# Performance work log

Measured on AMD Instinct MI355X. Metric: run time of the kernel, lower is better.

The kernel has to match this reference:

```python
import jax, jax.numpy as jnp
import numpy as np

D_K = 64

def setup_inputs() -> dict:
    key = jax.random.key(0)
    k1, k2, k3 = jax.random.split(key, 3)
    B, H, S, d = 4, 16, 2048, D_K
    Q = jax.random.normal(k1, (B, H, S, d), dtype=jnp.float32)
    K = jax.random.normal(k2, (B, H, S, d), dtype=jnp.float32)
    V = jax.random.normal(k3, (B, H, S, d), dtype=jnp.float32)
    attn_mask = jnp.ones((1, 1, S, S), dtype=jnp.float32)
    return {"Q": Q, "K": K, "V": V, "attn_mask": attn_mask}

def reference(Q, K, V, attn_mask):
    # scores = Q K^T / sqrt(d_k)  -> [B, H, S, S]
    scale = 1.0 / np.sqrt(D_K).astype(np.float32)
    scores = jnp.einsum('bhqd,bhkd->bhqk', Q, K) * scale
    # unnormalized exp (NO max-subtraction, faithful to original)
    scores = jnp.exp(scores)
    # multiplicative mask applied POST-exp
    scores = scores * attn_mask
    # manual sum-normalization with eps
    attn = scores / (jnp.sum(scores, axis=-1, keepdims=True) + 1e-08)
    context = jnp.einsum('bhqk,bhkd->bhqd', attn, V)
    return (context, attn)
```

## Files before the change

kernel.cpp:

```cpp
#include <hip/hip_runtime.h>

#define S_LEN 2048
#define D_KD  64
#define NKT   32
#define NBH   64

typedef __attribute__((ext_vector_type(8))) short short8;
typedef __attribute__((ext_vector_type(4))) float f32x4;

__device__ __forceinline__ unsigned short f2bf(float f) {
    unsigned u = __builtin_bit_cast(unsigned, f);
    return (unsigned short)((u + 0x7fffu + ((u >> 16) & 1u)) >> 16);
}

__device__ __forceinline__ unsigned swz(int row, int bytecol) {
    return (unsigned)(row * 128 + bytecol) ^
           (((((unsigned)row & 7u) ^ ((unsigned)row >> 3)) & 7u) << 4);
}

__device__ __forceinline__ void stage_rm(const float* __restrict__ g,
                                         unsigned char* lds, int tid) {
#pragma unroll
    for (int j = 0; j < 4; j++) {
        int idx = j * 1024 + tid * 4;
        int row = idx >> 6, col = idx & 63;
        float4 v = *(const float4*)(g + idx);
        ushort4 b = make_ushort4(f2bf(v.x), f2bf(v.y), f2bf(v.z), f2bf(v.w));
        *(ushort4*)(lds + swz(row, col * 2)) = b;
    }
}

__device__ __forceinline__ void stage_tr(const float* __restrict__ g,
                                         unsigned char* lds, int tid) {
#pragma unroll
    for (int j = 0; j < 4; j++) {
        int idx = j * 1024 + tid * 4;
        int row = idx >> 6, col = idx & 63;
        float4 v = *(const float4*)(g + idx);
        *(unsigned short*)(lds + swz(col + 0, row * 2)) = f2bf(v.x);
        *(unsigned short*)(lds + swz(col + 1, row * 2)) = f2bf(v.y);
        *(unsigned short*)(lds + swz(col + 2, row * 2)) = f2bf(v.z);
        *(unsigned short*)(lds + swz(col + 3, row * 2)) = f2bf(v.w);
    }
}

__device__ __forceinline__ void qkt(const unsigned char* Qs, const unsigned char* Ks,
                                    int wv, int lr, int lg, f32x4 acc[4]) {
    short8 a0 = *(const short8*)(Qs + swz(16 * wv + lr, 16 * lg));
    short8 a1 = *(const short8*)(Qs + swz(16 * wv + lr, 16 * lg + 64));
#pragma unroll
    for (int nt = 0; nt < 4; nt++) {
        short8 b0 = *(const short8*)(Ks + swz(16 * nt + lr, 16 * lg));
        short8 b1 = *(const short8*)(Ks + swz(16 * nt + lr, 16 * lg + 64));
        acc[nt] = __builtin_amdgcn_mfma_f32_16x16x32_bf16(a0, b0, acc[nt], 0, 0, 0);
        acc[nt] = __builtin_amdgcn_mfma_f32_16x16x32_bf16(a1, b1, acc[nt], 0, 0, 0);
    }
}

__global__ __launch_bounds__(256) void attn_fused(
    const float* __restrict__ Q, const float* __restrict__ K,
    const float* __restrict__ V, const float* __restrict__ M,
    float* __restrict__ out) {
    __shared__ unsigned char Qs[8192];
    __shared__ unsigned char Ks[8192];
    __shared__ unsigned char Vs[8192];
    __shared__ unsigned char Ps[8192];

    const int tid = threadIdx.x;
    const int wv = tid >> 6, lane = tid & 63, lr = lane & 15, lg = lane >> 4;
    const int qt = blockIdx.x & 31, bh = blockIdx.x >> 5;

    const float* Qg = Q + ((size_t)bh * S_LEN + qt * 64) * D_KD;
    const float* Kg = K + (size_t)bh * S_LEN * D_KD;
    const float* Vg = V + (size_t)bh * S_LEN * D_KD;
    float* ctxg = out + ((size_t)bh * S_LEN + qt * 64) * D_KD;
    float* attng = out + (size_t)NBH * S_LEN * D_KD +
                   (size_t)bh * S_LEN * S_LEN + (size_t)(qt * 64) * S_LEN;
    const float* Mg = M + (size_t)(qt * 64) * S_LEN;

    stage_rm(Qg, Qs, tid);

    f32x4 accc[4] = {};
    float rs[4] = {0.f, 0.f, 0.f, 0.f};

    for (int t = 0; t < NKT; t++) {
        stage_rm(Kg + (size_t)t * 64 * D_KD, Ks, tid);
        stage_tr(Vg + (size_t)t * 64 * D_KD, Vs, tid);
        __syncthreads();

        f32x4 acc[4] = {};
        qkt(Qs, Ks, wv, lr, lg, acc);

#pragma unroll
        for (int r = 0; r < 4; r++) {
            const int row = 16 * wv + 4 * lg + r;
            const float* mrow = Mg + (size_t)row * S_LEN + t * 64;
#pragma unroll
            for (int nt = 0; nt < 4; nt++) {
                float e = __expf(acc[nt][r] * 0.125f) * mrow[16 * nt + lr];
                rs[r] += e;
                *(unsigned short*)(Ps + swz(row, (16 * nt + lr) * 2)) = f2bf(e);
            }
        }
        __syncthreads();

#pragma unroll
        for (int kt = 0; kt < 2; kt++) {
            short8 pa = *(const short8*)(Ps + swz(16 * wv + lr, 16 * lg + 64 * kt));
#pragma unroll
            for (int nt = 0; nt < 4; nt++) {
                short8 vb = *(const short8*)(Vs + swz(16 * nt + lr, 16 * lg + 64 * kt));
                accc[nt] = __builtin_amdgcn_mfma_f32_16x16x32_bf16(pa, vb, accc[nt], 0, 0, 0);
            }
        }
        __syncthreads();
    }

    float inv[4];
#pragma unroll
    for (int r = 0; r < 4; r++) {
        float v = rs[r];
        v += __shfl_xor(v, 1);
        v += __shfl_xor(v, 2);
        v += __shfl_xor(v, 4);
        v += __shfl_xor(v, 8);
        inv[r] = 1.0f / (v + 1e-8f);
    }

#pragma unroll
    for (int r = 0; r < 4; r++) {
        const int row = 16 * wv + 4 * lg + r;
#pragma unroll
        for (int nt = 0; nt < 4; nt++)
            ctxg[(size_t)row * D_KD + 16 * nt + lr] = accc[nt][r] * inv[r];
    }

    for (int t = 0; t < NKT; t++) {
        __syncthreads();
        stage_rm(Kg + (size_t)t * 64 * D_KD, Ks, tid);
        __syncthreads();

        f32x4 acc[4] = {};
        qkt(Qs, Ks, wv, lr, lg, acc);

#pragma unroll
        for (int r = 0; r < 4; r++) {
            const int row = 16 * wv + 4 * lg + r;
            const float* mrow = Mg + (size_t)row * S_LEN + t * 64;
            float* arow = attng + (size_t)row * S_LEN + t * 64;
#pragma unroll
            for (int nt = 0; nt < 4; nt++) {
                float e = __expf(acc[nt][r] * 0.125f) * mrow[16 * nt + lr] * inv[r];
                __builtin_nontemporal_store(e, arow + 16 * nt + lr);
            }
        }
    }
}

extern "C" void kernel_launch(void* const* d_in, const int* in_sizes, int n_in,
                              void* d_out, int out_size, void* d_ws, size_t ws_size,
                              hipStream_t stream) {
    const float* Q = (const float*)d_in[0];
    const float* K = (const float*)d_in[1];
    const float* V = (const float*)d_in[2];
    const float* M = (const float*)d_in[3];
    float* out = (float*)d_out;
    attn_fused<<<dim3(NBH * 32), dim3(256), 0, stream>>>(Q, K, V, M, out);
}
```

Baseline: 518.7 us.

## Split attention into context and matrix kernels, spread attn writes over key segments

The fused kernel is split in two. The first kernel computes the context and the per-row normalizers and saves the inverse row sums to the workspace. The second kernel recomputes QK^T and writes the normalized attention matrix, with each key range split into 4 segments so it launches four times as many blocks for the write-heavy phase. The V transpose staging is also rewritten to load 4 rows and store packed ushort4 columns instead of scalar LDS writes. In exchange it adds a second launch, a workspace round-trip, and an extra Q staging per block.

After: 511.6 us. No clear change (-1.4%).

```diff
diff --git a/kernel.cpp b/kernel.cpp
--- a/kernel.cpp
+++ b/kernel.cpp
@@ -4,6 +4,7 @@
 #define D_KD  64
 #define NKT   32
 #define NBH   64
+#define KSEG  4
 
 typedef __attribute__((ext_vector_type(8))) short short8;
 typedef __attribute__((ext_vector_type(4))) float f32x4;
@@ -32,16 +33,22 @@
 
 __device__ __forceinline__ void stage_tr(const float* __restrict__ g,
                                          unsigned char* lds, int tid) {
-#pragma unroll
-    for (int j = 0; j < 4; j++) {
-        int idx = j * 1024 + tid * 4;
-        int row = idx >> 6, col = idx & 63;
-        float4 v = *(const float4*)(g + idx);
-        *(unsigned short*)(lds + swz(col + 0, row * 2)) = f2bf(v.x);
-        *(unsigned short*)(lds + swz(col + 1, row * 2)) = f2bf(v.y);
-        *(unsigned short*)(lds + swz(col + 2, row * 2)) = f2bf(v.z);
-        *(unsigned short*)(lds + swz(col + 3, row * 2)) = f2bf(v.w);
-    }
+    const int br = tid >> 4;
+    const int bc = tid & 15;
+    const float* gp = g + (4 * br) * 64 + 4 * bc;
+    float4 v0 = *(const float4*)(gp + 0 * 64);
+    float4 v1 = *(const float4*)(gp + 1 * 64);
+    float4 v2 = *(const float4*)(gp + 2 * 64);
+    float4 v3 = *(const float4*)(gp + 3 * 64);
+    ushort4 c;
+    c = make_ushort4(f2bf(v0.x), f2bf(v1.x), f2bf(v2.x), f2bf(v3.x));
+    *(ushort4*)(lds + swz(4 * bc + 0, 8 * br)) = c;
+    c = make_ushort4(f2bf(v0.y), f2bf(v1.y), f2bf(v2.y), f2bf(v3.y));
+    *(ushort4*)(lds + swz(4 * bc + 1, 8 * br)) = c;
+    c = make_ushort4(f2bf(v0.z), f2bf(v1.z), f2bf(v2.z), f2bf(v3.z));
+    *(ushort4*)(lds + swz(4 * bc + 2, 8 * br)) = c;
+    c = make_ushort4(f2bf(v0.w), f2bf(v1.w), f2bf(v2.w), f2bf(v3.w));
+    *(ushort4*)(lds + swz(4 * bc + 3, 8 * br)) = c;
 }
 
 __device__ __forceinline__ void qkt(const unsigned char* Qs, const unsigned char* Ks,
@@ -57,10 +64,10 @@
     }
 }
 
-__global__ __launch_bounds__(256) void attn_fused(
+__global__ __launch_bounds__(256) void attn_ctx(
     const float* __restrict__ Q, const float* __restrict__ K,
     const float* __restrict__ V, const float* __restrict__ M,
-    float* __restrict__ out) {
+    float* __restrict__ out, float* __restrict__ invg) {
     __shared__ unsigned char Qs[8192];
     __shared__ unsigned char Ks[8192];
     __shared__ unsigned char Vs[8192];
@@ -74,8 +81,6 @@
     const float* Kg = K + (size_t)bh * S_LEN * D_KD;
     const float* Vg = V + (size_t)bh * S_LEN * D_KD;
     float* ctxg = out + ((size_t)bh * S_LEN + qt * 64) * D_KD;
-    float* attng = out + (size_t)NBH * S_LEN * D_KD +
-                   (size_t)bh * S_LEN * S_LEN + (size_t)(qt * 64) * S_LEN;
     const float* Mg = M + (size_t)(qt * 64) * S_LEN;
 
     stage_rm(Qg, Qs, tid);
@@ -135,9 +140,44 @@
             ctxg[(size_t)row * D_KD + 16 * nt + lr] = accc[nt][r] * inv[r];
     }
 
-    for (int t = 0; t < NKT; t++) {
-        __syncthreads();
-        stage_rm(Kg + (size_t)t * 64 * D_KD, Ks, tid);
+    if (lr == 0) {
+#pragma unroll
+        for (int r = 0; r < 4; r++)
+            invg[(size_t)bh * S_LEN + qt * 64 + 16 * wv + 4 * lg + r] = inv[r];
+    }
+}
+
+__global__ __launch_bounds__(256) void attn_mat(
+    const float* __restrict__ Q, const float* __restrict__ K,
+    const float* __restrict__ M, const float* __restrict__ invg,
+    float* __restrict__ out) {
+    __shared__ unsigned char Qs[8192];
+    __shared__ unsigned char Ks[8192];
+
+    const int tid = threadIdx.x;
+    const int wv = tid >> 6, lane = tid & 63, lr = lane & 15, lg = lane >> 4;
+    const int ks = blockIdx.x & (KSEG - 1);
+    const int qt = (blockIdx.x >> 2) & 31;
+    const int bh = blockIdx.x >> 7;
+
+    const float* Qg = Q + ((size_t)bh * S_LEN + qt * 64) * D_KD;
+    const float* Kg = K + (size_t)bh * S_LEN * D_KD;
+    const float* Mg = M + (size_t)(qt * 64) * S_LEN;
+    float* attng = out + (size_t)NBH * S_LEN * D_KD +
+                   (size_t)bh * S_LEN * S_LEN + (size_t)(qt * 64) * S_LEN;
+
+    stage_rm(Qg, Qs, tid);
+
+    float inv[4];
+#pragma unroll
+    for (int r = 0; r < 4; r++)
+        inv[r] = invg[(size_t)bh * S_LEN + qt * 64 + 16 * wv + 4 * lg + r];
+
+    const int nt_kt = S_LEN / (64 * KSEG);
+    for (int kt = 0; kt < nt_kt; kt++) {
+        const int key0 = ks * (S_LEN / KSEG) + kt * 64;
+        if (kt) __syncthreads();
+        stage_rm(Kg + (size_t)key0 * D_KD, Ks, tid);
         __syncthreads();
 
         f32x4 acc[4] = {};
@@ -146,8 +186,8 @@
 #pragma unroll
         for (int r = 0; r < 4; r++) {
             const int row = 16 * wv + 4 * lg + r;
-            const float* mrow = Mg + (size_t)row * S_LEN + t * 64;
-            float* arow = attng + (size_t)row * S_LEN + t * 64;
+            const float* mrow = Mg + (size_t)row * S_LEN + key0;
+            float* arow = attng + (size_t)row * S_LEN + key0;
 #pragma unroll
             for (int nt = 0; nt < 4; nt++) {
                 float e = __expf(acc[nt][r] * 0.125f) * mrow[16 * nt + lr] * inv[r];
@@ -165,5 +205,7 @@
     const float* V = (const float*)d_in[2];
     const float* M = (const float*)d_in[3];
     float* out = (float*)d_out;
-    attn_fused<<<dim3(NBH * 32), dim3(256), 0, stream>>>(Q, K, V, M, out);
-}
+    float* invg = (float*)d_ws;
+    attn_ctx<<<dim3(NBH * 32), dim3(256), 0, stream>>>(Q, K, V, M, out, invg);
+    attn_mat<<<dim3(NBH * 32 * KSEG), dim3(256), 0, stream>>>(Q, K, M, invg, out);
+}
```
